# Kernel tuning notes

Measured on AMD Instinct MI355X. Metric: run time of the kernel, lower is better.

The kernel has to match this reference:

```python
import jax, jax.numpy as jnp
import numpy as np

N_STATE = 1024
N_HEAD = 16
B = 2
S = 2048


def setup_inputs() -> dict:
    key = jax.random.key(0)
    ks = jax.random.split(key, 8)
    s = 0.02
    x = jax.random.normal(ks[0], (B, S, N_STATE), dtype=jnp.float32)
    # causal additive mask, as in Whisper: upper triangle = -inf
    mask = jnp.where(jnp.triu(jnp.ones((S, S), dtype=bool), k=1), -jnp.inf, 0.0).astype(jnp.float32)
    Wq = jax.random.normal(ks[1], (N_STATE, N_STATE), dtype=jnp.float32) * s
    bq = jax.random.normal(ks[2], (N_STATE,), dtype=jnp.float32) * s
    Wk = jax.random.normal(ks[3], (N_STATE, N_STATE), dtype=jnp.float32) * s
    Wv = jax.random.normal(ks[4], (N_STATE, N_STATE), dtype=jnp.float32) * s
    bv = jax.random.normal(ks[5], (N_STATE,), dtype=jnp.float32) * s
    Wo = jax.random.normal(ks[6], (N_STATE, N_STATE), dtype=jnp.float32) * s
    bo = jax.random.normal(ks[7], (N_STATE,), dtype=jnp.float32) * s
    return {"x": x, "mask": mask, "Wq": Wq, "bq": bq, "Wk": Wk,
            "Wv": Wv, "bv": bv, "Wo": Wo, "bo": bo}


def reference(x, mask, Wq, bq, Wk, Wv, bv, Wo, bo):
    Bb, S_, D = x.shape
    H = N_HEAD
    hd = D // H
    scale = hd ** (-0.25)  # scale split across q and k, as in the source
    q = x @ Wq.T + bq              # [B,S,D]
    k = x @ Wk.T                   # key has no bias
    v = x @ Wv.T + bv
    # [B,S,D] -> [B,H,S,hd]
    q = q.reshape(Bb, S_, H, hd).transpose(0, 2, 1, 3) * scale
    k = k.reshape(Bb, S_, H, hd).transpose(0, 2, 1, 3) * scale
    v = v.reshape(Bb, S_, H, hd).transpose(0, 2, 1, 3)
    qk = jnp.einsum('bhsd,bhtd->bhst', q, k) + mask[:S_, :S_]
    w = jax.nn.softmax(qk, axis=-1).astype(q.dtype)
    out = jnp.einsum('bhst,bhtd->bhsd', w, v)
    out = out.transpose(0, 2, 1, 3).reshape(Bb, S_, D)
    return out @ Wo.T + bo
```

## Files before the change

### kernel.cpp

```cpp
#include <hip/hip_runtime.h>
#include <hip/hip_bf16.h>
#include <cmath>

typedef __bf16 bf16;
typedef __bf16 bf16x8 __attribute__((ext_vector_type(8)));
typedef __bf16 bf16x4 __attribute__((ext_vector_type(4)));
typedef float f32x4 __attribute__((ext_vector_type(4)));

#define QS 0.18033688f

__device__ __forceinline__ void load16_to_lds(const void* g, void* l) {
    __builtin_amdgcn_global_load_lds(
        (const __attribute__((address_space(1))) unsigned int*)g,
        (__attribute__((address_space(3))) unsigned int*)l, 16, 0, 0);
}

__global__ __launch_bounds__(256) void convert_kernel(
    const float* __restrict__ x,  const float* __restrict__ wq,
    const float* __restrict__ wk, const float* __restrict__ wv,
    const float* __restrict__ wo, bf16* __restrict__ dst)
{
    const size_t M1 = 1024ull * 1024ull, M4 = 4ull * M1;
    size_t i0 = ((size_t)blockIdx.x * 256 + threadIdx.x) * 8;
    const float* s;
    size_t off;
    float sc = 1.f;
    if      (i0 < M4)        { s = x;  off = i0; }
    else if (i0 < M4 + M1)   { s = wq; off = i0 - M4; sc = QS; }
    else if (i0 < M4 + 2*M1) { s = wk; off = i0 - M4 - M1; }
    else if (i0 < M4 + 3*M1) { s = wv; off = i0 - M4 - 2*M1; }
    else                     { s = wo; off = i0 - M4 - 3*M1; }
    float4 a = *(const float4*)(s + off);
    float4 b = *(const float4*)(s + off + 4);
    bf16x8 r = { (bf16)(a.x*sc), (bf16)(a.y*sc), (bf16)(a.z*sc), (bf16)(a.w*sc),
                 (bf16)(b.x*sc), (bf16)(b.y*sc), (bf16)(b.z*sc), (bf16)(b.w*sc) };
    *(bf16x8*)(dst + i0) = r;
}

template<int BM, int MODE>
__device__ __forceinline__ void gemm_core(
    const bf16* __restrict__ A, const bf16* __restrict__ W,
    const float* __restrict__ bias, void* __restrict__ C,
    int mb, int nb, float bias_scale)
{
    constexpr int IF = BM / 32;
    __shared__ __align__(16) bf16 As[BM * 32];
    __shared__ __align__(16) bf16 Bs[128 * 32];

    const int tid  = threadIdx.x;
    const int lane = tid & 63;
    const int wave = tid >> 6;
    const int wr   = (wave >> 1) * (BM / 2);
    const int wc   = (wave & 1) * 64;
    const int l15  = lane & 15;
    const int l4   = lane >> 4;
    const int swz  = (l4 ^ ((l15 >> 1) & 3)) * 8;

    f32x4 acc[IF][4] = {};

    for (int kt = 0; kt < 32; ++kt) {
#pragma unroll
        for (int it = 0; it < BM / 64; ++it) {
            int c = it * 256 + tid;
            int scol = ((c & 3) ^ ((c >> 3) & 3)) * 8;
            load16_to_lds(&A[(size_t)(mb * BM + (c >> 2)) * 1024 + kt * 32 + scol],
                          &As[(it * 256 + (tid & 192)) * 8]);
        }
#pragma unroll
        for (int it = 0; it < 2; ++it) {
            int c = it * 256 + tid;
            int scol = ((c & 3) ^ ((c >> 3) & 3)) * 8;
            load16_to_lds(&W[(size_t)(nb * 128 + (c >> 2)) * 1024 + kt * 32 + scol],
                          &Bs[(it * 256 + (tid & 192)) * 8]);
        }
        __syncthreads();
        bf16x8 af[IF], bfr[4];
#pragma unroll
        for (int i = 0; i < IF; ++i)
            af[i] = *(const bf16x8*)&As[(wr + i * 16 + l15) * 32 + swz];
#pragma unroll
        for (int j = 0; j < 4; ++j)
            bfr[j] = *(const bf16x8*)&Bs[(wc + j * 16 + l15) * 32 + swz];
#pragma unroll
        for (int i = 0; i < IF; ++i)
#pragma unroll
            for (int j = 0; j < 4; ++j)
                acc[i][j] = __builtin_amdgcn_mfma_f32_16x16x32_bf16(
                    af[i], bfr[j], acc[i][j], 0, 0, 0);
        __syncthreads();
    }

    if (MODE == 1 || MODE == 2) {
#pragma unroll
        for (int j = 0; j < 4; ++j) {
            int D = nb * 128 + wc + j * 16 + l15;
            float bv = bias ? bias[D] : 0.f;
            int hh = D >> 6, d = D & 63;
#pragma unroll
            for (int i = 0; i < IF; ++i) {
                int S0 = mb * BM + wr + i * 16 + l4 * 4;
#pragma unroll
                for (int r = 0; r < 4; ++r) {
                    int S = S0 + r;
                    int bb = S >> 11, key = S & 2047;
                    int bh = bb * 16 + hh, nt = key >> 6, ktl = key & 63;
                    size_t idx;
                    if (MODE == 1)
                        idx = ((size_t)(bh * 32 + nt) * 8 + (d >> 5) * 4 + (ktl >> 4)) * 512
                            + ((d >> 3) & 3) * 128 + (ktl & 15) * 8 + (d & 7);
                    else
                        idx = ((size_t)(bh * 32 + nt) * 8 + (ktl >> 5) * 4 + (d >> 4)) * 512
                            + ((ktl >> 3) & 3) * 128 + (d & 15) * 8 + (ktl & 7);
                    ((bf16*)C)[idx] = (bf16)(acc[i][j][r] + bv);
                }
            }
        }
    } else {
#pragma unroll
        for (int j = 0; j < 4; ++j) {
            int col = nb * 128 + wc + j * 16 + l15;
            float bv = bias ? bias[col] * bias_scale : 0.f;
#pragma unroll
            for (int i = 0; i < IF; ++i) {
                int row0 = mb * BM + wr + i * 16 + l4 * 4;
#pragma unroll
                for (int r = 0; r < 4; ++r) {
                    float val = acc[i][j][r] + bv;
                    size_t idx = (size_t)(row0 + r) * 1024 + col;
                    if (MODE == 3) ((float*)C)[idx] = val;
                    else           ((bf16*)C)[idx]  = (bf16)val;
                }
            }
        }
    }
}

__global__ __launch_bounds__(256) void qkv_kernel(
    const bf16* __restrict__ xb,
    const bf16* __restrict__ wqb, const float* __restrict__ bq,
    const bf16* __restrict__ wkb,
    const bf16* __restrict__ wvb, const float* __restrict__ bv,
    bf16* __restrict__ q, bf16* __restrict__ kfb, bf16* __restrict__ vfb)
{
    int mb = blockIdx.x;
    int nbg = blockIdx.y;
    int sel = nbg >> 3, nb = nbg & 7;
    if      (sel == 0) gemm_core<128, 0>(xb, wqb, bq,      q,   mb, nb, QS);
    else if (sel == 1) gemm_core<128, 1>(xb, wkb, nullptr, kfb, mb, nb, 1.f);
    else               gemm_core<128, 2>(xb, wvb, bv,      vfb, mb, nb, 1.f);
}

__global__ __launch_bounds__(256) void oproj_kernel(
    const bf16* __restrict__ ao, const bf16* __restrict__ wob,
    const float* __restrict__ bo, float* __restrict__ out)
{
    gemm_core<128, 3>(ao, wob, bo, out, blockIdx.x, blockIdx.y, 1.f);
}

__global__ __launch_bounds__(64, 4) void attn_kernel(
    const bf16* __restrict__ q, const bf16* __restrict__ kfb,
    const bf16* __restrict__ vfb, bf16* __restrict__ o,
    float* __restrict__ pbuf)
{
    __shared__ __align__(16) bf16 Ps[32 * 72];

    const int lane = threadIdx.x;
    const int l15  = lane & 15;
    const int l4   = lane >> 4;

    const int bh    = blockIdx.x;
    const int wt    = 63 - blockIdx.y;
    const int chunk = blockIdx.z;
    const int b  = bh >> 4, h = bh & 15;
    const int qrow0 = wt * 32;

    const int n   = (wt >> 1) + 1;
    const int nch = (n + 7) >> 3;
    if (chunk >= nch) return;
    const int nt0 = chunk * 8;
    const int nt1 = (nt0 + 8 < n) ? (nt0 + 8) : n;

    bf16x8 qf[2][2];
#pragma unroll
    for (int qb = 0; qb < 2; ++qb)
#pragma unroll
        for (int kk = 0; kk < 2; ++kk)
            qf[qb][kk] = *(const bf16x8*)&q[(size_t)(b * 2048 + qrow0 + qb * 16 + l15) * 1024
                                           + h * 64 + kk * 32 + l4 * 8];

    const bf16* kb = kfb + (size_t)bh * 131072;
    const bf16* vb = vfb + (size_t)bh * 131072;

    f32x4 oacc[2][4] = {};
    float lsum[2] = { 0.f, 0.f };

    for (int nt = nt0; nt < nt1; ++nt) {
        const bf16* kt_ = kb + nt * 4096;
        const bf16* vt_ = vb + nt * 4096;

        f32x4 s[2][4] = {};
#pragma unroll
        for (int kk = 0; kk < 2; ++kk) {
#pragma unroll
            for (int j = 0; j < 4; ++j) {
                bf16x8 kf = *(const bf16x8*)&kt_[(kk * 4 + j) * 512 + lane * 8];
                s[0][j] = __builtin_amdgcn_mfma_f32_16x16x32_bf16(kf, qf[0][kk], s[0][j], 0, 0, 0);
                s[1][j] = __builtin_amdgcn_mfma_f32_16x16x32_bf16(kf, qf[1][kk], s[1][j], 0, 0, 0);
            }
        }

        const bool diag = (nt == n - 1);
#pragma unroll
        for (int qb = 0; qb < 2; ++qb) {
            float pv[4][4];
            if (diag) {
                int qg = qrow0 + qb * 16 + l15;
#pragma unroll
                for (int j = 0; j < 4; ++j)
#pragma unroll
                    for (int r = 0; r < 4; ++r) {
                        int kg = nt * 64 + j * 16 + l4 * 4 + r;
                        pv[j][r] = (kg > qg) ? 0.f : __builtin_amdgcn_exp2f(s[qb][j][r]);
                    }
            } else {
#pragma unroll
                for (int j = 0; j < 4; ++j)
#pragma unroll
                    for (int r = 0; r < 4; ++r)
                        pv[j][r] = __builtin_amdgcn_exp2f(s[qb][j][r]);
            }
#pragma unroll
            for (int j = 0; j < 4; ++j)
                lsum[qb] += (pv[j][0] + pv[j][1]) + (pv[j][2] + pv[j][3]);

#pragma unroll
            for (int j = 0; j < 4; ++j) {
                bf16x4 pk = { (bf16)pv[j][0], (bf16)pv[j][1], (bf16)pv[j][2], (bf16)pv[j][3] };
                *(bf16x4*)&Ps[(qb * 16 + l15) * 72 + j * 16 + l4 * 4] = pk;
            }
        }

#pragma unroll
        for (int kk = 0; kk < 2; ++kk) {
            bf16x8 pf0 = *(const bf16x8*)&Ps[l15 * 72 + kk * 32 + l4 * 8];
            bf16x8 pf1 = *(const bf16x8*)&Ps[(16 + l15) * 72 + kk * 32 + l4 * 8];
#pragma unroll
            for (int f = 0; f < 4; ++f) {
                bf16x8 vf = *(const bf16x8*)&vt_[(kk * 4 + f) * 512 + lane * 8];
                oacc[0][f] = __builtin_amdgcn_mfma_f32_16x16x32_bf16(pf0, vf, oacc[0][f], 0, 0, 0);
                oacc[1][f] = __builtin_amdgcn_mfma_f32_16x16x32_bf16(pf1, vf, oacc[1][f], 0, 0, 0);
            }
        }
    }

    if (nch == 1) {
#pragma unroll
        for (int qb = 0; qb < 2; ++qb) {
            float ls = lsum[qb];
            ls += __shfl_xor(ls, 16, 64);
            ls += __shfl_xor(ls, 32, 64);
            float rinv[4];
#pragma unroll
            for (int r = 0; r < 4; ++r) rinv[r] = 1.f / __shfl(ls, l4 * 4 + r, 64);
#pragma unroll
            for (int f = 0; f < 4; ++f)
#pragma unroll
                for (int r = 0; r < 4; ++r)
                    o[(size_t)(b * 2048 + qrow0 + qb * 16 + l4 * 4 + r) * 1024 + h * 64 + f * 16 + l15]
                        = (bf16)(oacc[qb][f][r] * rinv[r]);
        }
    } else {
        float* ps = pbuf + ((size_t)(bh * 64 + wt) * 4 + chunk) * 2080;
#pragma unroll
        for (int qb = 0; qb < 2; ++qb) {
            float ls = lsum[qb];
            ls += __shfl_xor(ls, 16, 64);
            ls += __shfl_xor(ls, 32, 64);
            if (l4 == 0) ps[2048 + qb * 16 + l15] = ls;
#pragma unroll
            for (int f = 0; f < 4; ++f)
#pragma unroll
                for (int r = 0; r < 4; ++r)
                    ps[(qb * 16 + l4 * 4 + r) * 64 + f * 16 + l15] = oacc[qb][f][r];
        }
    }
}

__global__ __launch_bounds__(256) void combine_kernel(
    const float* __restrict__ pbuf, bf16* __restrict__ ao)
{
    const int bh = blockIdx.x;
    const int wt = 16 + blockIdx.y;
    const int b = bh >> 4, h = bh & 15;
    const int n   = (wt >> 1) + 1;
    const int nch = (n + 7) >> 3;

    const int tid = threadIdx.x;
    const int qq  = tid >> 3;
    const int d0  = (tid & 7) * 8;

    const float* base0 = pbuf + (size_t)(bh * 64 + wt) * 4 * 2080;

    float ls = 0.f;
    float acc[8] = {};
    for (int c = 0; c < nch; ++c) {
        const float* p = base0 + c * 2080;
        ls += p[2048 + qq];
        float4 a = *(const float4*)(p + qq * 64 + d0);
        float4 bb = *(const float4*)(p + qq * 64 + d0 + 4);
        acc[0] += a.x; acc[1] += a.y; acc[2] += a.z; acc[3] += a.w;
        acc[4] += bb.x; acc[5] += bb.y; acc[6] += bb.z; acc[7] += bb.w;
    }
    float inv = 1.f / ls;
    bf16x8 r = { (bf16)(acc[0]*inv), (bf16)(acc[1]*inv), (bf16)(acc[2]*inv), (bf16)(acc[3]*inv),
                 (bf16)(acc[4]*inv), (bf16)(acc[5]*inv), (bf16)(acc[6]*inv), (bf16)(acc[7]*inv) };
    *(bf16x8*)&ao[(size_t)(b * 2048 + wt * 32 + qq) * 1024 + h * 64 + d0] = r;
}

extern "C" void kernel_launch(void* const* d_in, const int* in_sizes, int n_in,
                              void* d_out, int out_size, void* d_ws, size_t ws_size,
                              hipStream_t stream)
{
    const float* x  = (const float*)d_in[0];
    const float* Wq = (const float*)d_in[2];
    const float* bq = (const float*)d_in[3];
    const float* Wk = (const float*)d_in[4];
    const float* Wv = (const float*)d_in[5];
    const float* bv = (const float*)d_in[6];
    const float* Wo = (const float*)d_in[7];
    const float* bo = (const float*)d_in[8];
    float* out = (float*)d_out;

    const size_t M1 = 1024ull * 1024ull, M4 = 4ull * M1;
    bf16* base = (bf16*)d_ws;
    bf16* xb  = base;
    bf16* wqb = base + M4;
    bf16* wkb = base + M4 + M1;
    bf16* wvb = base + M4 + 2 * M1;
    bf16* wob = base + M4 + 3 * M1;
    bf16* q   = base + 8 * M1;
    bf16* kfb = base + 12 * M1;
    bf16* vfb = base + 16 * M1;
    bf16* ao  = xb;
    float* pbuf = (float*)(base + 20 * M1);

    convert_kernel<<<4096, 256, 0, stream>>>(x, Wq, Wk, Wv, Wo, base);
    qkv_kernel<<<dim3(32, 24), 256, 0, stream>>>(xb, wqb, bq, wkb, wvb, bv, q, kfb, vfb);
    attn_kernel<<<dim3(32, 64, 4), 64, 0, stream>>>(q, kfb, vfb, ao, pbuf);
    combine_kernel<<<dim3(32, 48), 256, 0, stream>>>(pbuf, ao);
    oproj_kernel<<<dim3(32, 8), 256, 0, stream>>>(ao, wob, bo, out);
}
```

Before: 211.0 us.

## Double attention query tile to 64 rows per wave to reuse K/V loads

Each attention wave now handles 64 query rows instead of 32, so every K/V tile loaded from global memory feeds twice as many MFMAs. K and V fragments are loaded up front per tile, and the grid is flattened into a 2D layout with chunk in the low bits. The partial buffer and combine kernel are resized to match. In exchange register pressure roughly doubles (launch bounds lowered to 2 waves), there are half as many blocks, and the diagonal tile wastes more masked work.

```diff
diff --git a/kernel.cpp b/kernel.cpp
--- a/kernel.cpp
+++ b/kernel.cpp
@@ -157,32 +157,33 @@
     gemm_core<128, 3>(ao, wob, bo, out, blockIdx.x, blockIdx.y, 1.f);
 }
 
-__global__ __launch_bounds__(64, 4) void attn_kernel(
+__global__ __launch_bounds__(64, 2) void attn_kernel(
     const bf16* __restrict__ q, const bf16* __restrict__ kfb,
     const bf16* __restrict__ vfb, bf16* __restrict__ o,
     float* __restrict__ pbuf)
 {
-    __shared__ __align__(16) bf16 Ps[32 * 72];
+    __shared__ __align__(16) bf16 Ps[64 * 72];
 
     const int lane = threadIdx.x;
     const int l15  = lane & 15;
     const int l4   = lane >> 4;
 
     const int bh    = blockIdx.x;
-    const int wt    = 63 - blockIdx.y;
-    const int chunk = blockIdx.z;
+    const int yy    = blockIdx.y;
+    const int wt    = 31 - (yy >> 2);
+    const int chunk = yy & 3;
     const int b  = bh >> 4, h = bh & 15;
-    const int qrow0 = wt * 32;
-
-    const int n   = (wt >> 1) + 1;
+    const int qrow0 = wt * 64;
+
+    const int n   = wt + 1;
     const int nch = (n + 7) >> 3;
     if (chunk >= nch) return;
     const int nt0 = chunk * 8;
     const int nt1 = (nt0 + 8 < n) ? (nt0 + 8) : n;
 
-    bf16x8 qf[2][2];
-#pragma unroll
-    for (int qb = 0; qb < 2; ++qb)
+    bf16x8 qf[4][2];
+#pragma unroll
+    for (int qb = 0; qb < 4; ++qb)
 #pragma unroll
         for (int kk = 0; kk < 2; ++kk)
             qf[qb][kk] = *(const bf16x8*)&q[(size_t)(b * 2048 + qrow0 + qb * 16 + l15) * 1024
@@ -191,27 +192,33 @@
     const bf16* kb = kfb + (size_t)bh * 131072;
     const bf16* vb = vfb + (size_t)bh * 131072;
 
-    f32x4 oacc[2][4] = {};
-    float lsum[2] = { 0.f, 0.f };
+    f32x4 oacc[4][4] = {};
+    float lsum[4] = { 0.f, 0.f, 0.f, 0.f };
 
     for (int nt = nt0; nt < nt1; ++nt) {
         const bf16* kt_ = kb + nt * 4096;
         const bf16* vt_ = vb + nt * 4096;
 
-        f32x4 s[2][4] = {};
-#pragma unroll
-        for (int kk = 0; kk < 2; ++kk) {
+        bf16x8 kf[2][4], vf[2][4];
+#pragma unroll
+        for (int kk = 0; kk < 2; ++kk)
 #pragma unroll
             for (int j = 0; j < 4; ++j) {
-                bf16x8 kf = *(const bf16x8*)&kt_[(kk * 4 + j) * 512 + lane * 8];
-                s[0][j] = __builtin_amdgcn_mfma_f32_16x16x32_bf16(kf, qf[0][kk], s[0][j], 0, 0, 0);
-                s[1][j] = __builtin_amdgcn_mfma_f32_16x16x32_bf16(kf, qf[1][kk], s[1][j], 0, 0, 0);
-            }
-        }
+                kf[kk][j] = *(const bf16x8*)&kt_[(kk * 4 + j) * 512 + lane * 8];
+                vf[kk][j] = *(const bf16x8*)&vt_[(kk * 4 + j) * 512 + lane * 8];
+            }
 
         const bool diag = (nt == n - 1);
 #pragma unroll
-        for (int qb = 0; qb < 2; ++qb) {
+        for (int qb = 0; qb < 4; ++qb) {
+            f32x4 s[4] = {};
+#pragma unroll
+            for (int kk = 0; kk < 2; ++kk)
+#pragma unroll
+                for (int j = 0; j < 4; ++j)
+                    s[j] = __builtin_amdgcn_mfma_f32_16x16x32_bf16(
+                        kf[kk][j], qf[qb][kk], s[j], 0, 0, 0);
+
             float pv[4][4];
             if (diag) {
                 int qg = qrow0 + qb * 16 + l15;
@@ -220,14 +227,14 @@
 #pragma unroll
                     for (int r = 0; r < 4; ++r) {
                         int kg = nt * 64 + j * 16 + l4 * 4 + r;
-                        pv[j][r] = (kg > qg) ? 0.f : __builtin_amdgcn_exp2f(s[qb][j][r]);
+                        pv[j][r] = (kg > qg) ? 0.f : __builtin_amdgcn_exp2f(s[j][r]);
                     }
             } else {
 #pragma unroll
                 for (int j = 0; j < 4; ++j)
 #pragma unroll
                     for (int r = 0; r < 4; ++r)
-                        pv[j][r] = __builtin_amdgcn_exp2f(s[qb][j][r]);
+                        pv[j][r] = __builtin_amdgcn_exp2f(s[j][r]);
             }
 #pragma unroll
             for (int j = 0; j < 4; ++j)
@@ -242,20 +249,22 @@
 
 #pragma unroll
         for (int kk = 0; kk < 2; ++kk) {
-            bf16x8 pf0 = *(const bf16x8*)&Ps[l15 * 72 + kk * 32 + l4 * 8];
-            bf16x8 pf1 = *(const bf16x8*)&Ps[(16 + l15) * 72 + kk * 32 + l4 * 8];
-#pragma unroll
-            for (int f = 0; f < 4; ++f) {
-                bf16x8 vf = *(const bf16x8*)&vt_[(kk * 4 + f) * 512 + lane * 8];
-                oacc[0][f] = __builtin_amdgcn_mfma_f32_16x16x32_bf16(pf0, vf, oacc[0][f], 0, 0, 0);
-                oacc[1][f] = __builtin_amdgcn_mfma_f32_16x16x32_bf16(pf1, vf, oacc[1][f], 0, 0, 0);
-            }
+            bf16x8 pf[4];
+#pragma unroll
+            for (int qb = 0; qb < 4; ++qb)
+                pf[qb] = *(const bf16x8*)&Ps[(qb * 16 + l15) * 72 + kk * 32 + l4 * 8];
+#pragma unroll
+            for (int f = 0; f < 4; ++f)
+#pragma unroll
+                for (int qb = 0; qb < 4; ++qb)
+                    oacc[qb][f] = __builtin_amdgcn_mfma_f32_16x16x32_bf16(
+                        pf[qb], vf[kk][f], oacc[qb][f], 0, 0, 0);
         }
     }
 
     if (nch == 1) {
 #pragma unroll
-        for (int qb = 0; qb < 2; ++qb) {
+        for (int qb = 0; qb < 4; ++qb) {
             float ls = lsum[qb];
             ls += __shfl_xor(ls, 16, 64);
             ls += __shfl_xor(ls, 32, 64);
@@ -270,13 +279,13 @@
                         = (bf16)(oacc[qb][f][r] * rinv[r]);
         }
     } else {
-        float* ps = pbuf + ((size_t)(bh * 64 + wt) * 4 + chunk) * 2080;
-#pragma unroll
-        for (int qb = 0; qb < 2; ++qb) {
+        float* ps = pbuf + ((size_t)(bh * 32 + wt) * 4 + chunk) * 4160;
+#pragma unroll
+        for (int qb = 0; qb < 4; ++qb) {
             float ls = lsum[qb];
             ls += __shfl_xor(ls, 16, 64);
             ls += __shfl_xor(ls, 32, 64);
-            if (l4 == 0) ps[2048 + qb * 16 + l15] = ls;
+            if (l4 == 0) ps[4096 + qb * 16 + l15] = ls;
 #pragma unroll
             for (int f = 0; f < 4; ++f)
 #pragma unroll
@@ -290,31 +299,36 @@
     const float* __restrict__ pbuf, bf16* __restrict__ ao)
 {
     const int bh = blockIdx.x;
-    const int wt = 16 + blockIdx.y;
+    const int wt = 8 + blockIdx.y;
     const int b = bh >> 4, h = bh & 15;
-    const int n   = (wt >> 1) + 1;
+    const int n   = wt + 1;
     const int nch = (n + 7) >> 3;
 
     const int tid = threadIdx.x;
-    const int qq  = tid >> 3;
-    const int d0  = (tid & 7) * 8;
-
-    const float* base0 = pbuf + (size_t)(bh * 64 + wt) * 4 * 2080;
+    const int qq  = tid >> 2;
+    const int d0  = (tid & 3) * 16;
+
+    const float* base0 = pbuf + (size_t)(bh * 32 + wt) * 4 * 4160;
 
     float ls = 0.f;
-    float acc[8] = {};
+    float acc[16] = {};
     for (int c = 0; c < nch; ++c) {
-        const float* p = base0 + c * 2080;
-        ls += p[2048 + qq];
-        float4 a = *(const float4*)(p + qq * 64 + d0);
-        float4 bb = *(const float4*)(p + qq * 64 + d0 + 4);
-        acc[0] += a.x; acc[1] += a.y; acc[2] += a.z; acc[3] += a.w;
-        acc[4] += bb.x; acc[5] += bb.y; acc[6] += bb.z; acc[7] += bb.w;
+        const float* p = base0 + c * 4160;
+        ls += p[4096 + qq];
+#pragma unroll
+        for (int g = 0; g < 4; ++g) {
+            float4 a = *(const float4*)(p + qq * 64 + d0 + g * 4);
+            acc[g*4+0] += a.x; acc[g*4+1] += a.y; acc[g*4+2] += a.z; acc[g*4+3] += a.w;
+        }
     }
     float inv = 1.f / ls;
-    bf16x8 r = { (bf16)(acc[0]*inv), (bf16)(acc[1]*inv), (bf16)(acc[2]*inv), (bf16)(acc[3]*inv),
-                 (bf16)(acc[4]*inv), (bf16)(acc[5]*inv), (bf16)(acc[6]*inv), (bf16)(acc[7]*inv) };
-    *(bf16x8*)&ao[(size_t)(b * 2048 + wt * 32 + qq) * 1024 + h * 64 + d0] = r;
+    bf16* dst = &ao[(size_t)(b * 2048 + wt * 64 + qq) * 1024 + h * 64 + d0];
+    bf16x8 r0 = { (bf16)(acc[0]*inv), (bf16)(acc[1]*inv), (bf16)(acc[2]*inv), (bf16)(acc[3]*inv),
+                  (bf16)(acc[4]*inv), (bf16)(acc[5]*inv), (bf16)(acc[6]*inv), (bf16)(acc[7]*inv) };
+    bf16x8 r1 = { (bf16)(acc[8]*inv), (bf16)(acc[9]*inv), (bf16)(acc[10]*inv), (bf16)(acc[11]*inv),
+                  (bf16)(acc[12]*inv), (bf16)(acc[13]*inv), (bf16)(acc[14]*inv), (bf16)(acc[15]*inv) };
+    *(bf16x8*)dst = r0;
+    *(bf16x8*)(dst + 8) = r1;
 }
 
 extern "C" void kernel_launch(void* const* d_in, const int* in_sizes, int n_in,
@@ -346,7 +360,7 @@
 
     convert_kernel<<<4096, 256, 0, stream>>>(x, Wq, Wk, Wv, Wo, base);
     qkv_kernel<<<dim3(32, 24), 256, 0, stream>>>(xb, wqb, bq, wkb, wvb, bv, q, kfb, vfb);
-    attn_kernel<<<dim3(32, 64, 4), 64, 0, stream>>>(q, kfb, vfb, ao, pbuf);
-    combine_kernel<<<dim3(32, 48), 256, 0, stream>>>(pbuf, ao);
+    attn_kernel<<<dim3(32, 128), 64, 0, stream>>>(q, kfb, vfb, ao, pbuf);
+    combine_kernel<<<dim3(32, 24), 256, 0, stream>>>(pbuf, ao);
     oproj_kernel<<<dim3(32, 8), 256, 0, stream>>>(ao, wob, bo, out);
 }
```

After: 190.3 us. 9.8% less time.
